# Optimization experiments

Hardware: AMD Instinct MI355X
Metric: run time of the kernel (lower is better)

Reference implementation:

```python
import jax, jax.numpy as jnp
import numpy as np

B = 256
NUM_ROUTES = 32 * 6 * 6  # 1152
NUM_CAPS = 10
OUT_CH = 16
IN_CH = 8


def squash(x, axis=-1):
    sq = jnp.sum(x * x, axis=axis, keepdims=True)
    return sq * x / ((1.0 + sq) * jnp.sqrt(sq))


def conv2d(x, w, b, stride):
    y = jax.lax.conv_general_dilated(
        x, w, window_strides=(stride, stride), padding='VALID',
        dimension_numbers=('NCHW', 'OIHW', 'NCHW'))
    return y + b[None, :, None, None]


def setup_inputs() -> dict:
    key = jax.random.key(0)
    ks = jax.random.split(key, 12)
    data = jax.random.normal(ks[0], (B, 1, 28, 28), dtype=jnp.float32)
    conv1_w = jax.random.normal(ks[1], (256, 1, 9, 9), dtype=jnp.float32) * 0.1
    conv1_b = jax.random.normal(ks[2], (256,), dtype=jnp.float32) * 0.01
    # 8 primary-capsule convs, each 256->32, k9 s2 (stacked)
    pc_w = jax.random.normal(ks[3], (8, 32, 256, 9, 9), dtype=jnp.float32) * 0.02
    pc_b = jax.random.normal(ks[4], (8, 32), dtype=jnp.float32) * 0.01
    # DigitCaps routing weights (torch.randn init)
    W_dc = jax.random.normal(ks[5], (NUM_ROUTES, NUM_CAPS, OUT_CH, IN_CH), dtype=jnp.float32)
    dec_w1 = jax.random.normal(ks[6], (160, 512), dtype=jnp.float32) * 0.05
    dec_b1 = jnp.zeros((512,), dtype=jnp.float32)
    dec_w2 = jax.random.normal(ks[7], (512, 1024), dtype=jnp.float32) * 0.05
    dec_b2 = jnp.zeros((1024,), dtype=jnp.float32)
    dec_w3 = jax.random.normal(ks[8], (1024, 784), dtype=jnp.float32) * 0.05
    dec_b3 = jnp.zeros((784,), dtype=jnp.float32)
    return dict(data=data, conv1_w=conv1_w, conv1_b=conv1_b, pc_w=pc_w, pc_b=pc_b,
                W_dc=W_dc, dec_w1=dec_w1, dec_b1=dec_b1, dec_w2=dec_w2,
                dec_b2=dec_b2, dec_w3=dec_w3, dec_b3=dec_b3)


def capsnet_forward(data, conv1_w, conv1_b, pc_w, pc_b, W_dc,
                    dec_w1, dec_b1, dec_w2, dec_b2, dec_w3, dec_b3):
    bsz = data.shape[0]
    # ConvLayer: [B,1,28,28] -> [B,256,20,20]
    x = jax.nn.relu(conv2d(data, conv1_w, conv1_b, 1))
    # PrimaryCaps: 8 independent convs fused into one 256-out conv then split
    # [B,256,6,6] viewed as [B,8,32,6,6] matches torch.stack(u, dim=1)
    u = conv2d(x, pc_w.reshape(256, 256, 9, 9), pc_b.reshape(256), 2)
    u = u.reshape(bsz, NUM_ROUTES, IN_CH)  # [B,1152,8]
    u = squash(u)
    # DigitCaps: u_hat[b,r,c,o] = sum_i W[r,c,o,i] * u[b,r,i]
    u_hat = jnp.einsum('rcoi,bri->brco', W_dc, u)  # [B,1152,10,16]
    b_ij = jnp.zeros((NUM_ROUTES, NUM_CAPS), dtype=u_hat.dtype)
    num_iterations = 3
    v = None
    for it in range(num_iterations):
        c_ij = jax.nn.softmax(b_ij, axis=0)            # softmax over routes
        s_j = jnp.einsum('rc,brco->bco', c_ij, u_hat)  # [B,10,16]
        v = squash(s_j, axis=-1)
        if it < num_iterations - 1:
            a_ij = jnp.einsum('brco,bco->rc', u_hat, v) / bsz  # mean over batch
            b_ij = b_ij + a_ij
    output = v[..., None]  # [B,10,16,1]
    # Decoder
    classes = jnp.sqrt(jnp.sum(output ** 2, axis=2))   # [B,10,1]
    classes = jax.nn.softmax(classes, axis=0)          # softmax over batch (as in source)
    idx = jnp.argmax(classes, axis=1)[:, 0]            # [B]
    masked = jnp.eye(NUM_CAPS, dtype=output.dtype)[idx]  # [B,10]
    t = (output * masked[:, :, None, None]).reshape(bsz, -1)  # [B,160]
    h = jax.nn.relu(t @ dec_w1 + dec_b1)
    h = jax.nn.relu(h @ dec_w2 + dec_b2)
    recon = jax.nn.sigmoid(h @ dec_w3 + dec_b3).reshape(bsz, 1, 28, 28)
    return output, recon, masked


def reference(data, conv1_w, conv1_b, pc_w, pc_b, W_dc,
              dec_w1, dec_b1, dec_w2, dec_b2, dec_w3, dec_b3):
    return capsnet_forward(data, conv1_w, conv1_b, pc_w, pc_b, W_dc,
                           dec_w1, dec_b1, dec_w2, dec_b2, dec_w3, dec_b3)
```

## Files before the change

kernel.cpp:

```cpp
#include <hip/hip_runtime.h>
#include <math.h>


typedef __attribute__((ext_vector_type(8))) short short8;
typedef __attribute__((ext_vector_type(4))) float f32x4;

__device__ __forceinline__ unsigned short f2bf(float x) {
  unsigned int u = __float_as_uint(x);
  unsigned int r = (u + 0x7fffu + ((u >> 16) & 1u)) >> 16;
  return (unsigned short)r;
}
__device__ __forceinline__ float bf2f(unsigned short h) {
  return __uint_as_float(((unsigned int)h) << 16);
}
__device__ __forceinline__ void gload16(const void* g, void* l) {
  __builtin_amdgcn_global_load_lds(
      (const __attribute__((address_space(1))) unsigned int*)g,
      (__attribute__((address_space(3))) unsigned int*)l, 16, 0, 0);
}
__device__ __forceinline__ float dot8(const float* w, float4 a, float4 b) {
  return w[0]*a.x + w[1]*a.y + w[2]*a.z + w[3]*a.w +
         w[4]*b.x + w[5]*b.y + w[6]*b.z + w[7]*b.w;
}

__global__ __launch_bounds__(320) void conv1_kernel(
    const float* __restrict__ data, const float* __restrict__ w1,
    const float* __restrict__ b1, unsigned short* __restrict__ xh,
    unsigned short* __restrict__ xl)
{
  const int bid = blockIdx.x;
  const int b   = bid >> 2;
  const int cog = bid & 3;
  __shared__ float img[784];
  __shared__ float wsm[81][64];
  const int t = threadIdx.x;
  for (int i = t; i < 784; i += 320) img[i] = data[b * 784 + i];
  for (int i = t; i < 64 * 81; i += 320) {
    int col = i / 81, k = i % 81;
    wsm[k][col] = w1[(cog * 64 + col) * 81 + k];
  }
  __syncthreads();
  const int cg = t & 15;
  const int oy = t >> 4;
  const int co0 = cog * 64 + cg * 4;
  float acc[4][20];
  #pragma unroll
  for (int i = 0; i < 4; i++) {
    float bv = b1[co0 + i];
    #pragma unroll
    for (int j = 0; j < 20; j++) acc[i][j] = bv;
  }
  for (int ky = 0; ky < 9; ky++) {
    float xr[28];
    const float4* rp = reinterpret_cast<const float4*>(&img[(oy + ky) * 28]);
    #pragma unroll
    for (int q = 0; q < 7; q++) {
      float4 v4 = rp[q];
      xr[q*4+0] = v4.x; xr[q*4+1] = v4.y; xr[q*4+2] = v4.z; xr[q*4+3] = v4.w;
    }
    #pragma unroll
    for (int kx = 0; kx < 9; kx++) {
      float4 wv = *reinterpret_cast<const float4*>(&wsm[ky * 9 + kx][cg * 4]);
      #pragma unroll
      for (int ox = 0; ox < 20; ox++) {
        float xv = xr[ox + kx];
        acc[0][ox] = fmaf(xv, wv.x, acc[0][ox]);
        acc[1][ox] = fmaf(xv, wv.y, acc[1][ox]);
        acc[2][ox] = fmaf(xv, wv.z, acc[2][ox]);
        acc[3][ox] = fmaf(xv, wv.w, acc[3][ox]);
      }
    }
  }
  #pragma unroll
  for (int ox = 0; ox < 20; ox++) {
    ushort4 hv, lv;
    float v0 = fmaxf(acc[0][ox], 0.f), v1 = fmaxf(acc[1][ox], 0.f);
    float v2 = fmaxf(acc[2][ox], 0.f), v3 = fmaxf(acc[3][ox], 0.f);
    hv.x = f2bf(v0); lv.x = f2bf(v0 - bf2f(hv.x));
    hv.y = f2bf(v1); lv.y = f2bf(v1 - bf2f(hv.y));
    hv.z = f2bf(v2); lv.z = f2bf(v2 - bf2f(hv.z));
    hv.w = f2bf(v3); lv.w = f2bf(v3 - bf2f(hv.w));
    const int pix = (b * 20 + oy) * 20 + ox;
    *(ushort4*)(xh + pix * 256 + co0) = hv;
    *(ushort4*)(xl + pix * 256 + co0) = lv;
  }
}

__global__ void wprep(const float* __restrict__ pw, unsigned short* __restrict__ wh,
                      unsigned short* __restrict__ wl)
{
  const int co = blockIdx.x;
  const int t  = threadIdx.x;
  __shared__ float slab[20736];
  for (int i = t; i < 20736; i += 256) slab[i] = pw[co * 20736 + i];
  __syncthreads();
  const int cc = t >> 5, ci5 = t & 31;
  for (int k = 0; k < 81; k++) {
    float x = slab[t * 81 + k];
    unsigned short h = f2bf(x);
    int dst = ((k * 8 + cc) * 256 + co) * 32 + ci5;
    wh[dst] = h;
    wl[dst] = f2bf(x - bf2f(h));
  }
}

__global__ __launch_bounds__(256) void conv2_mfma(
    const unsigned short* __restrict__ xh, const unsigned short* __restrict__ xl,
    const unsigned short* __restrict__ wh, const unsigned short* __restrict__ wl,
    float* __restrict__ part)
{
  __shared__ char lds[49152];
  const int t   = threadIdx.x;
  const int blk = blockIdx.x;
  const int mt  = blk % 144;
  const int kg  = blk / 144;
  const int kyg = kg % 3;
  const int cih = kg / 3;
  const int m0  = mt * 64;
  const int lane = t & 63;
  const int w    = t >> 6;
  const int l15  = lane & 15, l4 = lane >> 4;

  const int g0  = t ^ ((t >> 3) & 7);
  const int ar0 = g0 >> 3;
  const int ach = g0 & 7;
  auto pixbase = [&](int pix) {
    int ab = pix / 36; int sp = pix - ab * 36;
    int oy = sp / 6;   int ox = sp - oy * 6;
    return ((ab * 20 + 2 * oy) * 20 + 2 * ox) * 256;
  };
  const int abase0 = pixbase(m0 + ar0) + ach * 8;
  const int abase1 = pixbase(m0 + ar0 + 32) + ach * 8;

  const int bofs = (w * 64 + l15) * 32 + l4 * 8;
  const int cibase = cih * 128;

  f32x4 acc[4][4];
  #pragma unroll
  for (int i = 0; i < 4; i++)
    #pragma unroll
    for (int j = 0; j < 4; j++) acc[i][j] = (f32x4){0.f, 0.f, 0.f, 0.f};

  const int ky0 = kyg * 3;

  auto stageA = [&](int buf, int xy, int ci0) {
    char* base = lds + buf * 16384;
    gload16(xh + abase0 + xy + ci0, base + t * 16);
    gload16(xh + abase1 + xy + ci0, base + 4096  + t * 16);
    gload16(xl + abase0 + xy + ci0, base + 8192  + t * 16);
    gload16(xl + abase1 + xy + ci0, base + 12288 + t * 16);
  };

  stageA(0, ky0 * 20 * 256, cibase);
  int kyc = ky0, kxc = 0, cc2 = 0;
  #pragma unroll 1
  for (int s = 0; s < 54; ++s) {
    const int kkc = (kyc * 9 + kxc) * 8 + cih * 4 + cc2 * 2;
    short8 b_h[4][2], b_l[4][2];
    #pragma unroll
    for (int ks = 0; ks < 2; ks++) {
      const unsigned short* bhp = wh + (kkc + ks) * 8192 + bofs;
      const unsigned short* blp = wl + (kkc + ks) * 8192 + bofs;
      #pragma unroll
      for (int nf = 0; nf < 4; nf++) {
        b_h[nf][ks] = *(const short8*)(bhp + nf * 512);
        b_l[nf][ks] = *(const short8*)(blp + nf * 512);
      }
    }
    cc2++; if (cc2 == 2) { cc2 = 0; kxc++; if (kxc == 9) { kxc = 0; kyc++; } }
    if (s < 53) {
      stageA((s + 1) % 3, (kyc * 20 + kxc) * 256, cibase + cc2 * 64);
      asm volatile("s_waitcnt vmcnt(20)" ::: "memory");
    } else {
      asm volatile("s_waitcnt vmcnt(16)" ::: "memory");
    }
    asm volatile("s_barrier" ::: "memory");

    char* base = lds + (s % 3) * 16384;
    #pragma unroll
    for (int ks = 0; ks < 2; ks++) {
      short8 a_h[4], a_l[4];
      #pragma unroll
      for (int mf = 0; mf < 4; mf++) {
        const int row = mf * 16 + l15;
        const int off = ((row * 8 + ks * 4 + l4) ^ (l15 & 7)) << 4;
        a_h[mf] = *(const short8*)(base + off);
        a_l[mf] = *(const short8*)(base + 8192 + off);
      }
      __builtin_amdgcn_s_setprio(1);
      #pragma unroll
      for (int nf = 0; nf < 4; nf++)
        #pragma unroll
        for (int mf = 0; mf < 4; mf++) {
          f32x4 a = acc[mf][nf];
          a = __builtin_amdgcn_mfma_f32_16x16x32_bf16(a_h[mf], b_h[nf][ks], a, 0, 0, 0);
          a = __builtin_amdgcn_mfma_f32_16x16x32_bf16(a_l[mf], b_h[nf][ks], a, 0, 0, 0);
          a = __builtin_amdgcn_mfma_f32_16x16x32_bf16(a_h[mf], b_l[nf][ks], a, 0, 0, 0);
          acc[mf][nf] = a;
        }
      __builtin_amdgcn_s_setprio(0);
    }
  }

  float* pout = part + kg * 2359296;
  #pragma unroll
  for (int mf = 0; mf < 4; mf++)
    #pragma unroll
    for (int nf = 0; nf < 4; nf++) {
      const int co = w * 64 + nf * 16 + l15;
      #pragma unroll
      for (int reg = 0; reg < 4; reg++) {
        const int pix = m0 + mf * 16 + l4 * 4 + reg;
        const int b  = pix / 36;
        const int sp = pix - b * 36;
        pout[b * 9216 + co * 36 + sp] = acc[mf][nf][reg];
      }
    }
}

__global__ void combine_squash(const float* __restrict__ part,
                               const float* __restrict__ pb,
                               float* __restrict__ uT)
{
  const int id = blockIdx.x * 256 + threadIdx.x;
  const int b = id / 1152;
  const int r = id % 1152;
  const float* p0 = part + b * 9216 + r * 8;
  float v[8];
  #pragma unroll
  for (int i = 0; i < 8; i++)
    v[i] = ((p0[i] + p0[2359296 + i]) + (p0[4718592 + i] + p0[7077888 + i]))
         + (p0[9437184 + i] + p0[11796480 + i]);
  #pragma unroll
  for (int i = 0; i < 8; i++) v[i] += pb[(r * 8 + i) / 36];
  float sq = 0.f;
  #pragma unroll
  for (int i = 0; i < 8; i++) sq += v[i] * v[i];
  float scale = sq / ((1.f + sq) * sqrtf(sq));
  #pragma unroll
  for (int i = 0; i < 8; i++) uT[(r * 256 + b) * 8 + i] = v[i] * scale;
}

__global__ __launch_bounds__(256) void s_pass(
    const float* __restrict__ uT, const float* __restrict__ Wdc,
    const float* __restrict__ bij, float* __restrict__ spart, int uniform)
{
  const int c  = blockIdx.x % 10;
  const int q  = blockIdx.x / 10;
  const int r0 = q * 18;
  const int t  = threadIdx.x;
  __shared__ float wsm[18 * 128];
  __shared__ float cw[18];
  __shared__ float red[8];

  #pragma unroll
  for (int k = 0; k < 9; k++) {
    int idx = t + k * 256;
    int r = idx >> 7, i = idx & 127;
    wsm[idx] = Wdc[((r0 + r) * 10 + c) * 128 + i];
  }
  if (uniform) {
    if (t < 18) cw[t] = 1.f / 1152.f;
  } else {
    float bv[5]; float m = -1e30f;
    #pragma unroll
    for (int rr = 0; rr < 5; rr++) {
      int r = t + rr * 256;
      bv[rr] = (r < 1152) ? bij[c * 1152 + r] : -1e30f;
      m = fmaxf(m, bv[rr]);
    }
    #pragma unroll
    for (int off = 32; off; off >>= 1) m = fmaxf(m, __shfl_down(m, off, 64));
    if ((t & 63) == 0) red[t >> 6] = m;
    __syncthreads();
    m = fmaxf(fmaxf(red[0], red[1]), fmaxf(red[2], red[3]));
    float ssum = 0.f;
    #pragma unroll
    for (int rr = 0; rr < 5; rr++)
      ssum += (t + rr * 256 < 1152) ? expf(bv[rr] - m) : 0.f;
    #pragma unroll
    for (int off = 32; off; off >>= 1) ssum += __shfl_down(ssum, off, 64);
    if ((t & 63) == 0) red[4 + (t >> 6)] = ssum;
    __syncthreads();
    float inv = 1.f / (red[4] + red[5] + red[6] + red[7]);
    if (t < 18) cw[t] = expf(bij[c * 1152 + r0 + t] - m) * inv;
  }
  __syncthreads();

  const float4* up = (const float4*)(uT + (r0 * 256 + t) * 8);
  float acc[16];
  #pragma unroll
  for (int o = 0; o < 16; o++) acc[o] = 0.f;
  #pragma unroll 1
  for (int r = 0; r < 18; r++) {
    float4 x0 = up[r * 512], x1 = up[r * 512 + 1];
    float cwr = cw[r];
    const float* wr = &wsm[r * 128];
    #pragma unroll
    for (int o = 0; o < 16; o++) {
      const float4 wa = *(const float4*)(wr + o * 8);
      const float4 wb = *(const float4*)(wr + o * 8 + 4);
      acc[o] += cwr * (wa.x*x0.x + wa.y*x0.y + wa.z*x0.z + wa.w*x0.w
                     + wb.x*x1.x + wb.y*x1.y + wb.z*x1.z + wb.w*x1.w);
    }
  }
  float* op = spart + q * 40960 + (t * 10 + c) * 16;
  #pragma unroll
  for (int o = 0; o < 16; o++) op[o] = acc[o];
}

template <int FINAL>
__global__ void reduce_squash(const float* __restrict__ spart, float* __restrict__ outb)
{
  const int id = blockIdx.x * 256 + threadIdx.x;
  float a = 0.f;
  #pragma unroll 8
  for (int q = 0; q < 64; q++) a += spart[q * 40960 + id];
  if (FINAL) { outb[id] = a; return; }
  float sq = a * a;
  #pragma unroll
  for (int off = 8; off; off >>= 1) sq += __shfl_xor(sq, off, 16);
  float scale = sq / ((1.f + sq) * sqrtf(sq));
  const int bc = id >> 4, o = id & 15;
  const int b = bc / 10, c = bc - b * 10;
  outb[(c * 256 + b) * 16 + o] = a * scale;
}

__global__ __launch_bounds__(256) void a_pass(
    const float* __restrict__ uT, const float* __restrict__ W,
    const float* __restrict__ vT, float* __restrict__ bij, int assign)
{
  const int r = blockIdx.x;
  const int t = threadIdx.x;
  __shared__ float wsl[1280];
  __shared__ float lred[4][10];
  for (int i = t; i < 1280; i += 256) wsl[i] = W[r * 1280 + i];
  __syncthreads();
  const float4* up = (const float4*)(uT + (r * 256 + t) * 8);
  float4 ua = up[0], ub = up[1];
  const int lane = t & 63, wid = t >> 6;
  #pragma unroll 1
  for (int c = 0; c < 10; c++) {
    const float* wc = &wsl[c * 128];
    const float4* vp = (const float4*)(vT + (c * 256 + t) * 16);
    float p = 0.f;
    #pragma unroll
    for (int q = 0; q < 4; q++) {
      float4 vq = vp[q];
      p += dot8(wc + (q * 4 + 0) * 8, ua, ub) * vq.x;
      p += dot8(wc + (q * 4 + 1) * 8, ua, ub) * vq.y;
      p += dot8(wc + (q * 4 + 2) * 8, ua, ub) * vq.z;
      p += dot8(wc + (q * 4 + 3) * 8, ua, ub) * vq.w;
    }
    for (int off = 32; off; off >>= 1) p += __shfl_down(p, off, 64);
    if (lane == 0) lred[wid][c] = p;
  }
  __syncthreads();
  if (t < 10) {
    float a = (lred[0][t] + lred[1][t] + lred[2][t] + lred[3][t]) * (1.f / 256.f);
    float o = assign ? 0.f : bij[t * 1152 + r];
    bij[t * 1152 + r] = o + a;
  }
}

__global__ __launch_bounds__(256) void finalize(
    const float* __restrict__ sbuf, float* __restrict__ outp,
    float* __restrict__ maskedo, float* __restrict__ tbuf)
{
  const int b = threadIdx.x;
  __shared__ float nsm[256][10];
  __shared__ float red[8];
  #pragma unroll 1
  for (int c = 0; c < 10; c++) {
    const float4* sp = (const float4*)(sbuf + (b * 10 + c) * 16);
    float4 q0 = sp[0], q1 = sp[1], q2 = sp[2], q3 = sp[3];
    float sq = q0.x*q0.x+q0.y*q0.y+q0.z*q0.z+q0.w*q0.w
             + q1.x*q1.x+q1.y*q1.y+q1.z*q1.z+q1.w*q1.w
             + q2.x*q2.x+q2.y*q2.y+q2.z*q2.z+q2.w*q2.w
             + q3.x*q3.x+q3.y*q3.y+q3.z*q3.z+q3.w*q3.w;
    float scale = sq / ((1.f + sq) * sqrtf(sq));
    float4* op = (float4*)(outp + (b * 10 + c) * 16);
    op[0] = make_float4(q0.x*scale, q0.y*scale, q0.z*scale, q0.w*scale);
    op[1] = make_float4(q1.x*scale, q1.y*scale, q1.z*scale, q1.w*scale);
    op[2] = make_float4(q2.x*scale, q2.y*scale, q2.z*scale, q2.w*scale);
    op[3] = make_float4(q3.x*scale, q3.y*scale, q3.z*scale, q3.w*scale);
    nsm[b][c] = sq / (1.f + sq);
  }
  __syncthreads();
  float sc[10];
  #pragma unroll
  for (int c = 0; c < 10; c++) {
    float x = nsm[b][c];
    float m = x;
    #pragma unroll
    for (int off = 32; off; off >>= 1) m = fmaxf(m, __shfl_down(m, off, 64));
    if ((b & 63) == 0) red[b >> 6] = m;
    __syncthreads();
    m = fmaxf(fmaxf(red[0], red[1]), fmaxf(red[2], red[3]));
    float e = expf(x - m), ss = e;
    #pragma unroll
    for (int off = 32; off; off >>= 1) ss += __shfl_down(ss, off, 64);
    if ((b & 63) == 0) red[4 + (b >> 6)] = ss;
    __syncthreads();
    sc[c] = e / (red[4] + red[5] + red[6] + red[7]);
    __syncthreads();
  }
  int idx = 0; float best = sc[0];
  #pragma unroll
  for (int c = 1; c < 10; c++) if (sc[c] > best) { best = sc[c]; idx = c; }
  #pragma unroll
  for (int c = 0; c < 10; c++) {
    float msk = (c == idx) ? 1.f : 0.f;
    maskedo[b * 10 + c] = msk;
    const float4* op = (const float4*)(outp + (b * 10 + c) * 16);
    float4* tp = (float4*)(tbuf + b * 160 + c * 16);
    #pragma unroll
    for (int qq = 0; qq < 4; qq++) {
      float4 vv = op[qq];
      tp[qq] = make_float4(vv.x * msk, vv.y * msk, vv.z * msk, vv.w * msk);
    }
  }
}

template <int ACT>
__global__ __launch_bounds__(256) void gemm_act(
    const float* __restrict__ A, const float* __restrict__ B,
    const float* __restrict__ bias, float* __restrict__ C, int M, int N, int K)
{
  __shared__ float As[64][17];
  __shared__ float Bs[16][64];
  const int t = threadIdx.x;
  const int tx = t & 15, ty = t >> 4;
  const int m0 = blockIdx.y * 64, n0 = blockIdx.x * 64;
  float acc[4][4] = {};
  for (int kb = 0; kb < K; kb += 16) {
    {
      int row = t >> 2, c4 = (t & 3) * 4;
      float4 av = *(const float4*)(A + (m0 + row) * K + kb + c4);
      As[row][c4+0]=av.x; As[row][c4+1]=av.y; As[row][c4+2]=av.z; As[row][c4+3]=av.w;
    }
    {
      int row = t >> 4, c4 = (t & 15) * 4;
      float4 bv = make_float4(0.f, 0.f, 0.f, 0.f);
      if (n0 + c4 < N) bv = *(const float4*)(B + (kb + row) * N + n0 + c4);
      Bs[row][c4+0]=bv.x; Bs[row][c4+1]=bv.y; Bs[row][c4+2]=bv.z; Bs[row][c4+3]=bv.w;
    }
    __syncthreads();
    #pragma unroll
    for (int kk = 0; kk < 16; kk++) {
      float a_[4], b_[4];
      #pragma unroll
      for (int i = 0; i < 4; i++) a_[i] = As[ty * 4 + i][kk];
      #pragma unroll
      for (int j = 0; j < 4; j++) b_[j] = Bs[kk][tx * 4 + j];
      #pragma unroll
      for (int i = 0; i < 4; i++)
        for (int j = 0; j < 4; j++)
          acc[i][j] = fmaf(a_[i], b_[j], acc[i][j]);
    }
    __syncthreads();
  }
  #pragma unroll
  for (int i = 0; i < 4; i++) {
    int row = m0 + ty * 4 + i;
    #pragma unroll
    for (int j = 0; j < 4; j++) {
      int col = n0 + tx * 4 + j;
      if (col < N) {
        float val = acc[i][j] + bias[col];
        if (ACT == 0) val = val > 0.f ? val : 0.f;
        else          val = 1.f / (1.f + expf(-val));
        C[row * N + col] = val;
      }
    }
  }
}

extern "C" void kernel_launch(void* const* d_in, const int* in_sizes, int n_in,
                              void* d_out, int out_size, void* d_ws, size_t ws_size,
                              hipStream_t stream)
{
  const float* data = (const float*)d_in[0];
  const float* w1   = (const float*)d_in[1];
  const float* b1   = (const float*)d_in[2];
  const float* pw   = (const float*)d_in[3];
  const float* pb   = (const float*)d_in[4];
  const float* Wdc  = (const float*)d_in[5];
  const float* dw1  = (const float*)d_in[6];
  const float* db1  = (const float*)d_in[7];
  const float* dw2  = (const float*)d_in[8];
  const float* db2  = (const float*)d_in[9];
  const float* dw3  = (const float*)d_in[10];
  const float* db3  = (const float*)d_in[11];

  float* out     = (float*)d_out;
  float* outp    = out;
  float* recon   = out + 40960;
  float* maskedo = out + 241664;

  char* wsb = (char*)d_ws;
  unsigned short* x1h = (unsigned short*)(wsb);
  unsigned short* x1l = (unsigned short*)(wsb + 52428800);
  unsigned short* wbh = (unsigned short*)(wsb + 104857600);
  unsigned short* wbl = (unsigned short*)(wsb + 115474432);
  float*  part = (float*)(wsb + 126091264);
  float* uT   = (float*)(wsb);
  float* vT   = (float*)(wsb + 9437184);
  float* bij  = (float*)(wsb + 9601024);
  float* sbuf = (float*)(wsb + 9647104);
  float* spart= (float*)(wsb + 9810944);
  float* tbuf = (float*)(wsb + 20296704);
  float* h1   = (float*)(wsb + 20460544);
  float* h2   = (float*)(wsb + 20984832);

  conv1_kernel<<<1024, 320, 0, stream>>>(data, w1, b1, x1h, x1l);
  wprep<<<256, 256, 0, stream>>>(pw, wbh, wbl);
  conv2_mfma<<<864, 256, 0, stream>>>(x1h, x1l, wbh, wbl, part);
  combine_squash<<<1152, 256, 0, stream>>>(part, pb, uT);

  s_pass<<<640, 256, 0, stream>>>(uT, Wdc, bij, spart, 1);
  reduce_squash<0><<<160, 256, 0, stream>>>(spart, vT);
  a_pass<<<1152, 256, 0, stream>>>(uT, Wdc, vT, bij, 1);
  s_pass<<<640, 256, 0, stream>>>(uT, Wdc, bij, spart, 0);
  reduce_squash<0><<<160, 256, 0, stream>>>(spart, vT);
  a_pass<<<1152, 256, 0, stream>>>(uT, Wdc, vT, bij, 0);
  s_pass<<<640, 256, 0, stream>>>(uT, Wdc, bij, spart, 0);
  reduce_squash<1><<<160, 256, 0, stream>>>(spart, sbuf);
  finalize<<<1, 256, 0, stream>>>(sbuf, outp, maskedo, tbuf);

  gemm_act<0><<<dim3(8, 4),  256, 0, stream>>>(tbuf, dw1, db1, h1,    256, 512,  160);
  gemm_act<0><<<dim3(16, 4), 256, 0, stream>>>(h1,   dw2, db2, h2,    256, 1024, 512);
  gemm_act<1><<<dim3(13, 4), 256, 0, stream>>>(h2,   dw3, db3, recon, 256, 784,  1024);
}
```

Baseline: 706.7 us.

## Move conv1 to bf16x3 MFMA and halve conv2 split-K partitions

Conv1 becomes an implicit-GEMM kernel on MFMA tensor instructions, using split bf16 hi/lo operands (three MFMAs per step) plus a small weight-transpose prep kernel. This replaces the scalar FMA direct convolution. Conv2 drops its split-K over input-channel halves, so each block now loops over all 256 channels (108 steps instead of 54). That halves the partial-sum buffers the combine kernel has to read, at the cost of fewer blocks (432) and less parallelism. The bf16x3 scheme drops the lo*lo term, which slightly changes conv1 precision.

After: 649.1 us (median of 2 runs). -8.1%, faster.

```diff
diff --git a/kernel.cpp b/kernel.cpp
--- a/kernel.cpp
+++ b/kernel.cpp
@@ -23,66 +23,94 @@
          w[4]*b.x + w[5]*b.y + w[6]*b.z + w[7]*b.w;
 }
 
-__global__ __launch_bounds__(320) void conv1_kernel(
-    const float* __restrict__ data, const float* __restrict__ w1,
-    const float* __restrict__ b1, unsigned short* __restrict__ xh,
-    unsigned short* __restrict__ xl)
-{
-  const int bid = blockIdx.x;
-  const int b   = bid >> 2;
-  const int cog = bid & 3;
-  __shared__ float img[784];
-  __shared__ float wsm[81][64];
-  const int t = threadIdx.x;
-  for (int i = t; i < 784; i += 320) img[i] = data[b * 784 + i];
-  for (int i = t; i < 64 * 81; i += 320) {
-    int col = i / 81, k = i % 81;
-    wsm[k][col] = w1[(cog * 64 + col) * 81 + k];
-  }
+__global__ void w1prep(const float* __restrict__ w1,
+                       unsigned short* __restrict__ w1th,
+                       unsigned short* __restrict__ w1tl)
+{
+  const int k  = blockIdx.x;
+  const int co = threadIdx.x;
+  float x = (k < 81) ? w1[co * 81 + k] : 0.f;
+  unsigned short h = f2bf(x);
+  w1th[co * 96 + k] = h;
+  w1tl[co * 96 + k] = f2bf(x - bf2f(h));
+}
+
+__global__ __launch_bounds__(256) void conv1_mfma(
+    const float* __restrict__ data, const unsigned short* __restrict__ w1th,
+    const unsigned short* __restrict__ w1tl, const float* __restrict__ b1,
+    unsigned short* __restrict__ xh, unsigned short* __restrict__ xl)
+{
+  __shared__ float img[1344];
+  __shared__ int offt[96];
+  const int t   = threadIdx.x;
+  const int b   = blockIdx.x >> 1;
+  const int coh = blockIdx.x & 1;
+  const int lane = t & 63, w = t >> 6;
+  const int l15 = lane & 15, l4 = lane >> 4;
+
+  for (int i = t; i < 1344; i += 256) img[i] = (i < 784) ? data[b * 784 + i] : 0.f;
+  if (t < 96) offt[t] = (t < 81) ? ((t / 9) * 28 + (t % 9)) : 784;
   __syncthreads();
-  const int cg = t & 15;
-  const int oy = t >> 4;
-  const int co0 = cog * 64 + cg * 4;
-  float acc[4][20];
-  #pragma unroll
-  for (int i = 0; i < 4; i++) {
-    float bv = b1[co0 + i];
-    #pragma unroll
-    for (int j = 0; j < 20; j++) acc[i][j] = bv;
-  }
-  for (int ky = 0; ky < 9; ky++) {
-    float xr[28];
-    const float4* rp = reinterpret_cast<const float4*>(&img[(oy + ky) * 28]);
-    #pragma unroll
-    for (int q = 0; q < 7; q++) {
-      float4 v4 = rp[q];
-      xr[q*4+0] = v4.x; xr[q*4+1] = v4.y; xr[q*4+2] = v4.z; xr[q*4+3] = v4.w;
-    }
-    #pragma unroll
-    for (int kx = 0; kx < 9; kx++) {
-      float4 wv = *reinterpret_cast<const float4*>(&wsm[ky * 9 + kx][cg * 4]);
-      #pragma unroll
-      for (int ox = 0; ox < 20; ox++) {
-        float xv = xr[ox + kx];
-        acc[0][ox] = fmaf(xv, wv.x, acc[0][ox]);
-        acc[1][ox] = fmaf(xv, wv.y, acc[1][ox]);
-        acc[2][ox] = fmaf(xv, wv.z, acc[2][ox]);
-        acc[3][ox] = fmaf(xv, wv.w, acc[3][ox]);
-      }
-    }
-  }
-  #pragma unroll
-  for (int ox = 0; ox < 20; ox++) {
-    ushort4 hv, lv;
-    float v0 = fmaxf(acc[0][ox], 0.f), v1 = fmaxf(acc[1][ox], 0.f);
-    float v2 = fmaxf(acc[2][ox], 0.f), v3 = fmaxf(acc[3][ox], 0.f);
-    hv.x = f2bf(v0); lv.x = f2bf(v0 - bf2f(hv.x));
-    hv.y = f2bf(v1); lv.y = f2bf(v1 - bf2f(hv.y));
-    hv.z = f2bf(v2); lv.z = f2bf(v2 - bf2f(hv.z));
-    hv.w = f2bf(v3); lv.w = f2bf(v3 - bf2f(hv.w));
-    const int pix = (b * 20 + oy) * 20 + ox;
-    *(ushort4*)(xh + pix * 256 + co0) = hv;
-    *(ushort4*)(xl + pix * 256 + co0) = lv;
+
+  short8 bh[3][2], bl[3][2];
+  #pragma unroll
+  for (int ks = 0; ks < 3; ks++)
+    #pragma unroll
+    for (int nf = 0; nf < 2; nf++) {
+      const int co = coh * 128 + w * 32 + nf * 16 + l15;
+      bh[ks][nf] = *(const short8*)(w1th + co * 96 + ks * 32 + l4 * 8);
+      bl[ks][nf] = *(const short8*)(w1tl + co * 96 + ks * 32 + l4 * 8);
+    }
+  int koff[3][8];
+  #pragma unroll
+  for (int ks = 0; ks < 3; ks++)
+    #pragma unroll
+    for (int j = 0; j < 8; j++)
+      koff[ks][j] = offt[ks * 32 + l4 * 8 + j];
+  float bv[2];
+  bv[0] = b1[coh * 128 + w * 32 + l15];
+  bv[1] = b1[coh * 128 + w * 32 + 16 + l15];
+
+  #pragma unroll 1
+  for (int mf = 0; mf < 25; mf++) {
+    const int p  = mf * 16 + l15;
+    const int oy = p / 20, ox = p - oy * 20;
+    const int base = oy * 28 + ox;
+    f32x4 acc[2];
+    acc[0] = (f32x4){0.f, 0.f, 0.f, 0.f};
+    acc[1] = (f32x4){0.f, 0.f, 0.f, 0.f};
+    #pragma unroll
+    for (int ks = 0; ks < 3; ks++) {
+      short8 ah, al;
+      #pragma unroll
+      for (int j = 0; j < 8; j++) {
+        float a = img[base + koff[ks][j]];
+        unsigned short h = f2bf(a);
+        ah[j] = (short)h;
+        al[j] = (short)f2bf(a - bf2f(h));
+      }
+      #pragma unroll
+      for (int nf = 0; nf < 2; nf++) {
+        f32x4 a4 = acc[nf];
+        a4 = __builtin_amdgcn_mfma_f32_16x16x32_bf16(ah, bh[ks][nf], a4, 0, 0, 0);
+        a4 = __builtin_amdgcn_mfma_f32_16x16x32_bf16(al, bh[ks][nf], a4, 0, 0, 0);
+        a4 = __builtin_amdgcn_mfma_f32_16x16x32_bf16(ah, bl[ks][nf], a4, 0, 0, 0);
+        acc[nf] = a4;
+      }
+    }
+    #pragma unroll
+    for (int nf = 0; nf < 2; nf++) {
+      const int co = coh * 128 + w * 32 + nf * 16 + l15;
+      #pragma unroll
+      for (int reg = 0; reg < 4; reg++) {
+        const int p2 = mf * 16 + l4 * 4 + reg;
+        float v = fmaxf(acc[nf][reg] + bv[nf], 0.f);
+        unsigned short h = f2bf(v);
+        const int pix = b * 400 + p2;
+        xh[pix * 256 + co] = h;
+        xl[pix * 256 + co] = f2bf(v - bf2f(h));
+      }
+    }
   }
 }
 
@@ -114,8 +142,6 @@
   const int blk = blockIdx.x;
   const int mt  = blk % 144;
   const int kg  = blk / 144;
-  const int kyg = kg % 3;
-  const int cih = kg / 3;
   const int m0  = mt * 64;
   const int lane = t & 63;
   const int w    = t >> 6;
@@ -133,7 +159,6 @@
   const int abase1 = pixbase(m0 + ar0 + 32) + ach * 8;
 
   const int bofs = (w * 64 + l15) * 32 + l4 * 8;
-  const int cibase = cih * 128;
 
   f32x4 acc[4][4];
   #pragma unroll
@@ -141,7 +166,7 @@
     #pragma unroll
     for (int j = 0; j < 4; j++) acc[i][j] = (f32x4){0.f, 0.f, 0.f, 0.f};
 
-  const int ky0 = kyg * 3;
+  const int ky0 = kg * 3;
 
   auto stageA = [&](int buf, int xy, int ci0) {
     char* base = lds + buf * 16384;
@@ -151,11 +176,11 @@
     gload16(xl + abase1 + xy + ci0, base + 12288 + t * 16);
   };
 
-  stageA(0, ky0 * 20 * 256, cibase);
+  stageA(0, ky0 * 20 * 256, 0);
   int kyc = ky0, kxc = 0, cc2 = 0;
   #pragma unroll 1
-  for (int s = 0; s < 54; ++s) {
-    const int kkc = (kyc * 9 + kxc) * 8 + cih * 4 + cc2 * 2;
+  for (int s = 0; s < 108; ++s) {
+    const int kkc = (kyc * 9 + kxc) * 8 + cc2 * 2;
     short8 b_h[4][2], b_l[4][2];
     #pragma unroll
     for (int ks = 0; ks < 2; ks++) {
@@ -167,9 +192,9 @@
         b_l[nf][ks] = *(const short8*)(blp + nf * 512);
       }
     }
-    cc2++; if (cc2 == 2) { cc2 = 0; kxc++; if (kxc == 9) { kxc = 0; kyc++; } }
-    if (s < 53) {
-      stageA((s + 1) % 3, (kyc * 20 + kxc) * 256, cibase + cc2 * 64);
+    cc2++; if (cc2 == 4) { cc2 = 0; kxc++; if (kxc == 9) { kxc = 0; kyc++; } }
+    if (s < 107) {
+      stageA((s + 1) % 3, (kyc * 20 + kxc) * 256, cc2 * 64);
       asm volatile("s_waitcnt vmcnt(20)" ::: "memory");
     } else {
       asm volatile("s_waitcnt vmcnt(16)" ::: "memory");
@@ -228,9 +253,7 @@
   const float* p0 = part + b * 9216 + r * 8;
   float v[8];
   #pragma unroll
-  for (int i = 0; i < 8; i++)
-    v[i] = ((p0[i] + p0[2359296 + i]) + (p0[4718592 + i] + p0[7077888 + i]))
-         + (p0[9437184 + i] + p0[11796480 + i]);
+  for (int i = 0; i < 8; i++) v[i] = p0[i] + p0[2359296 + i] + p0[4718592 + i];
   #pragma unroll
   for (int i = 0; i < 8; i++) v[i] += pb[(r * 8 + i) / 36];
   float sq = 0.f;
@@ -504,6 +527,8 @@
   unsigned short* wbh = (unsigned short*)(wsb + 104857600);
   unsigned short* wbl = (unsigned short*)(wsb + 115474432);
   float*  part = (float*)(wsb + 126091264);
+  unsigned short* w1th = (unsigned short*)(wsb + 154402816);
+  unsigned short* w1tl = (unsigned short*)(wsb + 154451968);
   float* uT   = (float*)(wsb);
   float* vT   = (float*)(wsb + 9437184);
   float* bij  = (float*)(wsb + 9601024);
@@ -513,9 +538,10 @@
   float* h1   = (float*)(wsb + 20460544);
   float* h2   = (float*)(wsb + 20984832);
 
-  conv1_kernel<<<1024, 320, 0, stream>>>(data, w1, b1, x1h, x1l);
+  w1prep<<<96, 256, 0, stream>>>(w1, w1th, w1tl);
+  conv1_mfma<<<512, 256, 0, stream>>>(data, w1th, w1tl, b1, x1h, x1l);
   wprep<<<256, 256, 0, stream>>>(pw, wbh, wbl);
-  conv2_mfma<<<864, 256, 0, stream>>>(x1h, x1l, wbh, wbl, part);
+  conv2_mfma<<<432, 256, 0, stream>>>(x1h, x1l, wbh, wbl, part);
   combine_squash<<<1152, 256, 0, stream>>>(part, pb, uT);
 
   s_pass<<<640, 256, 0, stream>>>(uT, Wdc, bij, spart, 1);
```
